# Kernel optimization log

Measured on AMD Instinct MI355X. Metric: run time of the kernel, lower is better.

## Reference

```python
import jax, jax.numpy as jnp
import numpy as np
from jax import lax

K = 2048  # nb_subsampled_points


def setup_inputs() -> dict:
    key = jax.random.key(0)
    k1, k2 = jax.random.split(key)
    B, N, D = 32, 131072, 3
    x = jax.random.normal(k1, (B, N, D), dtype=jnp.float32)
    start_idx = jax.random.randint(k2, (B,), 0, N, dtype=jnp.int64)
    return {"x": x, "start_idx": start_idx}


def reference(x, start_idx):
    """Iterative farthest point sampling.

    x: [B, N, D] point cloud, start_idx: [B] initial centroid indices.
    Returns [B, K] int indices of the sampled centroids.
    """
    B, N, D = x.shape

    def step(carry, _):
        min_d, idx = carry                                   # [B,N], [B]
        centroid = jnp.take_along_axis(x, idx[:, None, None], axis=1)  # [B,1,D]
        dist = jnp.sqrt(jnp.sum((x - centroid) ** 2, axis=2))          # [B,N]
        min_d = jnp.minimum(min_d, dist)
        next_idx = jnp.argmax(min_d, axis=1)                 # farthest point
        return (min_d, next_idx), idx

    init = (jnp.full((B, N), jnp.inf, dtype=x.dtype), start_idx.astype(jnp.int32))
    _, idxs = lax.scan(step, init, None, length=K)           # [K, B]
    return idxs.T                                            # [B, K]
```

## Files before the change

kernel.cpp:

```cpp
#include <hip/hip_runtime.h>

#define NB 32
#define NPTS 131072
#define KSAMP 2048
#define NPART 8
#define TPB 512
#define NPT 32
#define PART_PTS (NPTS / NPART)


#define RPT32(X) X(0)X(1)X(2)X(3)X(4)X(5)X(6)X(7)X(8)X(9)X(10)X(11)X(12) \
  X(13)X(14)X(15)X(16)X(17)X(18)X(19)X(20)X(21)X(22)X(23)X(24)X(25)X(26) \
  X(27)X(28)X(29)X(30)X(31)

__global__ __launch_bounds__(TPB)
__attribute__((amdgpu_waves_per_eu(2, 2)))
void fps_kernel(
    const float* __restrict__ x, const int* __restrict__ start,
    int* __restrict__ out, unsigned long long* __restrict__ slot)
{
  #pragma clang fp contract(off)
  const int blk  = blockIdx.x;
  const int xcd  = blk & 7;
  const int j    = blk >> 3;
  const int b    = xcd * 4 + (j & 3);
  const int part = j >> 2;
  const int tid  = threadIdx.x;
  const int lane = tid & 63;
  const int wave = tid >> 6;

  const float* xb = x + (size_t)b * (NPTS * 3);

  bool is64 = true;
  #pragma unroll 1
  for (int i = 1; i < 32; i += 2) {
    if (start[i] != 0) { is64 = false; break; }
  }
  int cur = is64 ? start[2 * b] : start[b];

  const int base = part * PART_PTS + tid;

  #define DECLP(J) float px##J, py##J, pz##J, md2##J;
  RPT32(DECLP)
  #define INITP(J) { const int n = base + (J) * TPB;          \
      px##J = xb[3*n]; py##J = xb[3*n+1]; pz##J = xb[3*n+2];  \
      md2##J = __builtin_inff(); }
  RPT32(INITP)
  #define PINP(J) asm("" : "+v"(px##J), "+v"(py##J), "+v"(pz##J));
  RPT32(PINP)

  __shared__ unsigned long long wred[TPB / 64];
  __shared__ int snext;

  if (part == 0 && tid == 0) out[b * KSAMP] = cur;

  float cx = xb[3 * (size_t)cur + 0];
  float cy = xb[3 * (size_t)cur + 1];
  float cz = xb[3 * (size_t)cur + 2];

  unsigned long long* const srow0 = slot + (size_t)b * 2 * NPART;

  for (int k = 0; k < KSAMP - 1; ++k) {
    float bestv = -1.0f;
    int   bestn = 0;
    #define SCANP(J) {                                              \
      const float dx = px##J - cx;                                  \
      const float dy = py##J - cy;                                  \
      const float dz = pz##J - cz;                                  \
      const float d2 = fmaf(dz, dz, fmaf(dx, dx, dy * dy));         \
      const float m  = fminf(md2##J, d2);                           \
      md2##J = m;                                                   \
      if (m > bestv) { bestv = m; bestn = base + (J) * TPB; }       \
    }
    RPT32(SCANP)

    const float sdw = sqrtf(bestv);

    unsigned long long key =
        ((unsigned long long)__float_as_uint(sdw) << 32) |
        (unsigned int)(NPTS - 1 - bestn);

    #pragma unroll
    for (int off = 32; off >= 1; off >>= 1) {
      unsigned long long o = __shfl_xor(key, off, 64);
      if (o > key) key = o;
    }
    if (lane == 0) wred[wave] = key;
    __syncthreads();

    if (wave == 0) {
      unsigned long long v = wred[lane & 7];
      #pragma unroll
      for (int off = 4; off >= 1; off >>= 1) {
        unsigned long long o = __shfl_xor(v, off, 64);
        if (o > v) v = o;
      }

      const unsigned tag = (unsigned)(k + 1);
      unsigned long long* const row = srow0 + (unsigned)(k & 1) * NPART;
      if (lane == 0)
        __hip_atomic_store(&row[part], v | ((unsigned long long)tag << 17),
                           __ATOMIC_RELAXED, __HIP_MEMORY_SCOPE_AGENT);

      unsigned long long g;
      do {
        g = __hip_atomic_load(&row[lane & (NPART - 1)], __ATOMIC_RELAXED,
                              __HIP_MEMORY_SCOPE_AGENT);
      } while (__ballot(((unsigned)(g >> 17) & 0x7FFFu) == tag) != ~0ull);

      #pragma unroll
      for (int off = 4; off >= 1; off >>= 1) {
        unsigned long long o = __shfl_xor(g, off, 64);
        if (o > g) g = o;
      }
      const int nidx = NPTS - 1 - (int)(g & 0x1FFFFu);
      if (lane == 0) {
        snext = nidx;
        if (part == 0) out[b * KSAMP + k + 1] = nidx;
      }
    }
    __syncthreads();

    const int nidx = snext;
    cx = xb[3 * (size_t)nidx + 0];
    cy = xb[3 * (size_t)nidx + 1];
    cz = xb[3 * (size_t)nidx + 2];
  }
}

extern "C" void kernel_launch(void* const* d_in, const int* in_sizes, int n_in,
                              void* d_out, int out_size, void* d_ws, size_t ws_size,
                              hipStream_t stream) {
  const float* x     = (const float*)d_in[0];
  const int*   start = (const int*)d_in[1];
  int*         out   = (int*)d_out;
  unsigned long long* slot = (unsigned long long*)d_ws;

  void* args[] = {(void*)&x, (void*)&start, (void*)&out, (void*)&slot};
  hipLaunchCooperativeKernel((void*)fps_kernel, dim3(NB * NPART), dim3(TPB),
                             args, 0, stream);
}
```

Measured before the change: 4.649 ms.

## Split each batch over 16 blocks with 16 points per thread

Adds a variant kernel that divides each batch's points across 16 cooperative blocks instead of 8. Each thread then holds 16 points in registers, which shortens the serial scan per iteration and allows more blocks per CU. The host queries occupancy and falls back to the original 8-part kernel if two blocks cannot fit per CU. The cost is a cross-block barrier spanning twice as many participants and an extra shuffle stage on every iteration, plus the removal of the register-pinning asm.

```diff
diff --git a/kernel.cpp b/kernel.cpp
--- a/kernel.cpp
+++ b/kernel.cpp
@@ -3,19 +3,41 @@
 #define NB 32
 #define NPTS 131072
 #define KSAMP 2048
-#define NPART 8
 #define TPB 512
-#define NPT 32
-#define PART_PTS (NPTS / NPART)
-
-
-#define RPT32(X) X(0)X(1)X(2)X(3)X(4)X(5)X(6)X(7)X(8)X(9)X(10)X(11)X(12) \
-  X(13)X(14)X(15)X(16)X(17)X(18)X(19)X(20)X(21)X(22)X(23)X(24)X(25)X(26) \
-  X(27)X(28)X(29)X(30)X(31)
-
-__global__ __launch_bounds__(TPB)
-__attribute__((amdgpu_waves_per_eu(2, 2)))
-void fps_kernel(
+
+
+#define RPT16(X) X(0)X(1)X(2)X(3)X(4)X(5)X(6)X(7)X(8)X(9)X(10)X(11)X(12) \
+  X(13)X(14)X(15)
+#define RPT32(X) RPT16(X) X(16)X(17)X(18)X(19)X(20)X(21)X(22)X(23)X(24) \
+  X(25)X(26)X(27)X(28)X(29)X(30)X(31)
+
+#define DECLP(J) float px##J, py##J, pz##J, md2##J;
+#define INITP(J) { const int n = base + (J) * TPB;          \
+    px##J = xb[3*n]; py##J = xb[3*n+1]; pz##J = xb[3*n+2];  \
+    md2##J = __builtin_inff(); }
+#define SCANP(J) {                                              \
+    const float dx = px##J - cx;                                \
+    const float dy = py##J - cy;                                \
+    const float dz = pz##J - cz;                                \
+    const float d2 = fmaf(dz, dz, fmaf(dx, dx, dy * dy));       \
+    const float m  = fminf(md2##J, d2);                         \
+    md2##J = m;                                                 \
+    if (m > bestv) { bestv = m; bestn = base + (J) * TPB; }     \
+  }
+
+__device__ __forceinline__ int read_start(const int* start, int b) {
+  bool is64 = true;
+  #pragma unroll 1
+  for (int i = 1; i < 32; i += 2) {
+    if (start[i] != 0) { is64 = false; break; }
+  }
+  return is64 ? start[2 * b] : start[b];
+}
+
+#define NPART16 16
+#define PART_PTS16 (NPTS / NPART16)
+
+__global__ __launch_bounds__(TPB, 4) void fps_kernel16(
     const float* __restrict__ x, const int* __restrict__ start,
     int* __restrict__ out, unsigned long long* __restrict__ slot)
 {
@@ -30,24 +52,11 @@
   const int wave = tid >> 6;
 
   const float* xb = x + (size_t)b * (NPTS * 3);
-
-  bool is64 = true;
-  #pragma unroll 1
-  for (int i = 1; i < 32; i += 2) {
-    if (start[i] != 0) { is64 = false; break; }
-  }
-  int cur = is64 ? start[2 * b] : start[b];
-
-  const int base = part * PART_PTS + tid;
-
-  #define DECLP(J) float px##J, py##J, pz##J, md2##J;
-  RPT32(DECLP)
-  #define INITP(J) { const int n = base + (J) * TPB;          \
-      px##J = xb[3*n]; py##J = xb[3*n+1]; pz##J = xb[3*n+2];  \
-      md2##J = __builtin_inff(); }
-  RPT32(INITP)
-  #define PINP(J) asm("" : "+v"(px##J), "+v"(py##J), "+v"(pz##J));
-  RPT32(PINP)
+  int cur = read_start(start, b);
+  const int base = part * PART_PTS16 + tid;
+
+  RPT16(DECLP)
+  RPT16(INITP)
 
   __shared__ unsigned long long wred[TPB / 64];
   __shared__ int snext;
@@ -58,21 +67,12 @@
   float cy = xb[3 * (size_t)cur + 1];
   float cz = xb[3 * (size_t)cur + 2];
 
-  unsigned long long* const srow0 = slot + (size_t)b * 2 * NPART;
+  unsigned long long* const srow0 = slot + (size_t)b * 2 * NPART16;
 
   for (int k = 0; k < KSAMP - 1; ++k) {
     float bestv = -1.0f;
     int   bestn = 0;
-    #define SCANP(J) {                                              \
-      const float dx = px##J - cx;                                  \
-      const float dy = py##J - cy;                                  \
-      const float dz = pz##J - cz;                                  \
-      const float d2 = fmaf(dz, dz, fmaf(dx, dx, dy * dy));         \
-      const float m  = fminf(md2##J, d2);                           \
-      md2##J = m;                                                   \
-      if (m > bestv) { bestv = m; bestn = base + (J) * TPB; }       \
-    }
-    RPT32(SCANP)
+    RPT16(SCANP)
 
     const float sdw = sqrtf(bestv);
 
@@ -97,14 +97,110 @@
       }
 
       const unsigned tag = (unsigned)(k + 1);
-      unsigned long long* const row = srow0 + (unsigned)(k & 1) * NPART;
+      unsigned long long* const row = srow0 + (unsigned)(k & 1) * NPART16;
       if (lane == 0)
         __hip_atomic_store(&row[part], v | ((unsigned long long)tag << 17),
                            __ATOMIC_RELAXED, __HIP_MEMORY_SCOPE_AGENT);
 
       unsigned long long g;
       do {
-        g = __hip_atomic_load(&row[lane & (NPART - 1)], __ATOMIC_RELAXED,
+        g = __hip_atomic_load(&row[lane & (NPART16 - 1)], __ATOMIC_RELAXED,
+                              __HIP_MEMORY_SCOPE_AGENT);
+      } while (__ballot(((unsigned)(g >> 17) & 0x7FFFu) == tag) != ~0ull);
+
+      #pragma unroll
+      for (int off = 8; off >= 1; off >>= 1) {
+        unsigned long long o = __shfl_xor(g, off, 64);
+        if (o > g) g = o;
+      }
+      const int nidx = NPTS - 1 - (int)(g & 0x1FFFFu);
+      if (lane == 0) {
+        snext = nidx;
+        if (part == 0) out[b * KSAMP + k + 1] = nidx;
+      }
+    }
+    __syncthreads();
+
+    const int nidx = snext;
+    cx = xb[3 * (size_t)nidx + 0];
+    cy = xb[3 * (size_t)nidx + 1];
+    cz = xb[3 * (size_t)nidx + 2];
+  }
+}
+
+#define NPART32 8
+#define PART_PTS32 (NPTS / NPART32)
+
+__global__ __launch_bounds__(TPB)
+__attribute__((amdgpu_waves_per_eu(2, 2)))
+void fps_kernel32(
+    const float* __restrict__ x, const int* __restrict__ start,
+    int* __restrict__ out, unsigned long long* __restrict__ slot)
+{
+  #pragma clang fp contract(off)
+  const int blk  = blockIdx.x;
+  const int xcd  = blk & 7;
+  const int j    = blk >> 3;
+  const int b    = xcd * 4 + (j & 3);
+  const int part = j >> 2;
+  const int tid  = threadIdx.x;
+  const int lane = tid & 63;
+  const int wave = tid >> 6;
+
+  const float* xb = x + (size_t)b * (NPTS * 3);
+  int cur = read_start(start, b);
+  const int base = part * PART_PTS32 + tid;
+
+  RPT32(DECLP)
+  RPT32(INITP)
+
+  __shared__ unsigned long long wred[TPB / 64];
+  __shared__ int snext;
+
+  if (part == 0 && tid == 0) out[b * KSAMP] = cur;
+
+  float cx = xb[3 * (size_t)cur + 0];
+  float cy = xb[3 * (size_t)cur + 1];
+  float cz = xb[3 * (size_t)cur + 2];
+
+  unsigned long long* const srow0 = slot + (size_t)b * 2 * NPART32;
+
+  for (int k = 0; k < KSAMP - 1; ++k) {
+    float bestv = -1.0f;
+    int   bestn = 0;
+    RPT32(SCANP)
+
+    const float sdw = sqrtf(bestv);
+
+    unsigned long long key =
+        ((unsigned long long)__float_as_uint(sdw) << 32) |
+        (unsigned int)(NPTS - 1 - bestn);
+
+    #pragma unroll
+    for (int off = 32; off >= 1; off >>= 1) {
+      unsigned long long o = __shfl_xor(key, off, 64);
+      if (o > key) key = o;
+    }
+    if (lane == 0) wred[wave] = key;
+    __syncthreads();
+
+    if (wave == 0) {
+      unsigned long long v = wred[lane & 7];
+      #pragma unroll
+      for (int off = 4; off >= 1; off >>= 1) {
+        unsigned long long o = __shfl_xor(v, off, 64);
+        if (o > v) v = o;
+      }
+
+      const unsigned tag = (unsigned)(k + 1);
+      unsigned long long* const row = srow0 + (unsigned)(k & 1) * NPART32;
+      if (lane == 0)
+        __hip_atomic_store(&row[part], v | ((unsigned long long)tag << 17),
+                           __ATOMIC_RELAXED, __HIP_MEMORY_SCOPE_AGENT);
+
+      unsigned long long g;
+      do {
+        g = __hip_atomic_load(&row[lane & (NPART32 - 1)], __ATOMIC_RELAXED,
                               __HIP_MEMORY_SCOPE_AGENT);
       } while (__ballot(((unsigned)(g >> 17) & 0x7FFFu) == tag) != ~0ull);
 
@@ -137,6 +233,15 @@
   unsigned long long* slot = (unsigned long long*)d_ws;
 
   void* args[] = {(void*)&x, (void*)&start, (void*)&out, (void*)&slot};
-  hipLaunchCooperativeKernel((void*)fps_kernel, dim3(NB * NPART), dim3(TPB),
-                             args, 0, stream);
-}
+
+  int occ = 0;
+  (void)hipOccupancyMaxActiveBlocksPerMultiprocessor(
+      &occ, (const void*)fps_kernel16, TPB, 0);
+  if (occ >= 2) {
+    hipLaunchCooperativeKernel((void*)fps_kernel16, dim3(NB * NPART16),
+                               dim3(TPB), args, 0, stream);
+  } else {
+    hipLaunchCooperativeKernel((void*)fps_kernel32, dim3(NB * NPART32),
+                               dim3(TPB), args, 0, stream);
+  }
+}
```

Measured after the change: 4.644 ms. Within noise of the previous version (-0.1%).

## Replace block barriers with per-wave global slot exchange for argmax

Applied to the files above, without the earlier changes.

Each wave now publishes its own argmax key to a global slot (64 per batch) and every wave polls all 64 slots itself, removing the LDS staging and both __syncthreads per iteration. The intent is to cut intra-block barrier latency from the serial FPS loop. In exchange every wave spins on global atomics, which adds memory traffic and poll contention. The register-pinning asm is also dropped.

```diff
diff --git a/kernel.cpp b/kernel.cpp
--- a/kernel.cpp
+++ b/kernel.cpp
@@ -7,6 +7,8 @@
 #define TPB 512
 #define NPT 32
 #define PART_PTS (NPTS / NPART)
+#define BATCH_F (NPTS * 3)
+#define NWAVE 64
 
 
 #define RPT32(X) X(0)X(1)X(2)X(3)X(4)X(5)X(6)X(7)X(8)X(9)X(10)X(11)X(12) \
@@ -28,8 +30,9 @@
   const int tid  = threadIdx.x;
   const int lane = tid & 63;
   const int wave = tid >> 6;
+  const int gid  = part * 8 + wave;
 
-  const float* xb = x + (size_t)b * (NPTS * 3);
+  const float* xb = x + (size_t)b * BATCH_F;
 
   bool is64 = true;
   #pragma unroll 1
@@ -46,11 +49,6 @@
       px##J = xb[3*n]; py##J = xb[3*n+1]; pz##J = xb[3*n+2];  \
       md2##J = __builtin_inff(); }
   RPT32(INITP)
-  #define PINP(J) asm("" : "+v"(px##J), "+v"(py##J), "+v"(pz##J));
-  RPT32(PINP)
-
-  __shared__ unsigned long long wred[TPB / 64];
-  __shared__ int snext;
 
   if (part == 0 && tid == 0) out[b * KSAMP] = cur;
 
@@ -58,7 +56,7 @@
   float cy = xb[3 * (size_t)cur + 1];
   float cz = xb[3 * (size_t)cur + 2];
 
-  unsigned long long* const srow0 = slot + (size_t)b * 2 * NPART;
+  unsigned long long* const srow0 = slot + (size_t)b * 2 * NWAVE;
 
   for (int k = 0; k < KSAMP - 1; ++k) {
     float bestv = -1.0f;
@@ -85,43 +83,27 @@
       unsigned long long o = __shfl_xor(key, off, 64);
       if (o > key) key = o;
     }
-    if (lane == 0) wred[wave] = key;
-    __syncthreads();
 
-    if (wave == 0) {
-      unsigned long long v = wred[lane & 7];
-      #pragma unroll
-      for (int off = 4; off >= 1; off >>= 1) {
-        unsigned long long o = __shfl_xor(v, off, 64);
-        if (o > v) v = o;
-      }
+    const unsigned tag = (unsigned)(k + 1);
+    unsigned long long* const row = srow0 + (unsigned)(k & 1) * NWAVE;
+    if (lane == 0)
+      __hip_atomic_store(&row[gid], key | ((unsigned long long)tag << 17),
+                         __ATOMIC_RELAXED, __HIP_MEMORY_SCOPE_AGENT);
 
-      const unsigned tag = (unsigned)(k + 1);
-      unsigned long long* const row = srow0 + (unsigned)(k & 1) * NPART;
-      if (lane == 0)
-        __hip_atomic_store(&row[part], v | ((unsigned long long)tag << 17),
-                           __ATOMIC_RELAXED, __HIP_MEMORY_SCOPE_AGENT);
+    unsigned long long g;
+    do {
+      g = __hip_atomic_load(&row[lane], __ATOMIC_RELAXED,
+                            __HIP_MEMORY_SCOPE_AGENT);
+    } while (__ballot(((unsigned)(g >> 17) & 0x7FFFu) == tag) != ~0ull);
 
-      unsigned long long g;
-      do {
-        g = __hip_atomic_load(&row[lane & (NPART - 1)], __ATOMIC_RELAXED,
-                              __HIP_MEMORY_SCOPE_AGENT);
-      } while (__ballot(((unsigned)(g >> 17) & 0x7FFFu) == tag) != ~0ull);
+    #pragma unroll
+    for (int off = 32; off >= 1; off >>= 1) {
+      unsigned long long o = __shfl_xor(g, off, 64);
+      if (o > g) g = o;
+    }
+    const int nidx = NPTS - 1 - (int)(g & 0x1FFFFu);
+    if (gid == 0 && lane == 0) out[b * KSAMP + k + 1] = nidx;
 
-      #pragma unroll
-      for (int off = 4; off >= 1; off >>= 1) {
-        unsigned long long o = __shfl_xor(g, off, 64);
-        if (o > g) g = o;
-      }
-      const int nidx = NPTS - 1 - (int)(g & 0x1FFFFu);
-      if (lane == 0) {
-        snext = nidx;
-        if (part == 0) out[b * KSAMP + k + 1] = nidx;
-      }
-    }
-    __syncthreads();
-
-    const int nidx = snext;
     cx = xb[3 * (size_t)nidx + 0];
     cy = xb[3 * (size_t)nidx + 1];
     cz = xb[3 * (size_t)nidx + 2];
```

Result: slower. 13.78 ms (+196.5%).
